# Performance work log

Measured on AMD Instinct MI355X. Metric: run time of the kernel, lower is better.

## Reference

```python
import jax, jax.numpy as jnp
import numpy as np

B, L, E, H = 8, 2048, 1024, 16
D = E // H
EPS = 1e-6


def setup_inputs() -> dict:
    key = jax.random.key(0)
    ks = jax.random.split(key, 9)
    s = 1.0 / np.sqrt(E)
    def lin_w(k):
        return jax.random.uniform(k, (E, E), jnp.float32, -s, s)
    def lin_b(k):
        return jax.random.uniform(k, (E,), jnp.float32, -s, s)
    return {
        "query": jax.random.normal(ks[0], (B, L, E), jnp.float32),
        "Wq": lin_w(ks[1]), "bq": lin_b(ks[2]),
        "Wk": lin_w(ks[3]), "bk": lin_b(ks[4]),
        "Wv": lin_w(ks[5]), "bv": lin_b(ks[6]),
        "Wo": lin_w(ks[7]), "bo": lin_b(ks[8]),
    }


def reference(query, Wq, bq, Wk, bk, Wv, bv, Wo, bo):
    bsz, tgt_len, embed_dim = query.shape
    n_head = H
    head_dim = embed_dim // n_head
    m = tgt_len  # src_len == tgt_len (self-attention)

    # projections (torch Linear with W stored as (in, out) here)
    q = query @ Wq + bq
    k = query @ Wk + bk
    v = query @ Wv + bv

    # (B, L, E) -> (B, H, L, D), softmax feature map over head dim
    def to_heads(x):
        return x.reshape(bsz, tgt_len, n_head, head_dim).transpose(0, 2, 1, 3)

    q = jax.nn.softmax(to_heads(q), axis=-1)
    k = jax.nn.softmax(to_heads(k), axis=-1)
    v = to_heads(v)
    comp_q = 1.0 - q
    comp_k = 1.0 - k

    # cosFormer positional reweighting: idx = (pi/2) * (1..m) / m
    idx = (np.pi / 2) * jnp.arange(1, m + 1, dtype=jnp.float32) / m  # (L,)
    sin = jnp.sin(idx)[None, None, :, None]  # (1,1,L,1)
    cos = jnp.cos(idx)[None, None, :, None]

    def feat(x):  # (B,H,L,D) -> (B,H,L,2D)
        return jnp.concatenate([x * sin, x * cos], axis=-1)

    qf, comp_qf = feat(q), feat(comp_q)
    kf, comp_kf = feat(k), feat(comp_k)

    def branch(qf_, kf_):
        kv = jnp.einsum('bhld,bhlm->bhdm', kf_, v)            # (B,H,2D,D)
        z = 1.0 / jnp.maximum(
            jnp.einsum('bhld,bhd->bhl', qf_, kf_.sum(axis=2)), EPS)
        return jnp.einsum('bhld,bhdm,bhl->bhlm', qf_, kv, z)  # (B,H,L,D)

    attn = branch(qf, kf) + branch(comp_qf, comp_kf)

    # torch: (B*H,L,D).transpose(0,1).view(L,B,E)
    out = attn.transpose(2, 0, 1, 3).reshape(tgt_len, bsz, embed_dim)
    out = out @ Wo + bo
    # torch final: .view(bsz, tgt_len, n_feat) -- raw reshape, no transpose
    return out.reshape(bsz, tgt_len, embed_dim)
```

## Files before the change

### kernel.cpp

```cpp
#include <hip/hip_runtime.h>
#include <hip/hip_bf16.h>
#include <cstdint>

#define B_   8
#define L_   2048
#define E_   1024
#define H_   16
#define D_   64
#define M_   (B_ * L_)
#define EPS_ 1e-6f
#define PI2_ 1.57079632679f

typedef __bf16 bf16;
typedef __bf16 bf16x8 __attribute__((ext_vector_type(8)));
typedef __bf16 bf16x4 __attribute__((ext_vector_type(4)));
typedef float  floatx4 __attribute__((ext_vector_type(4)));

__device__ inline void async_cp16(const void* g, void* l) {
  __builtin_amdgcn_global_load_lds(
      (__attribute__((address_space(1))) void*)const_cast<void*>(g),
      (__attribute__((address_space(3))) void*)l,
      16, 0, 0);
}

__global__ __launch_bounds__(256) void k_convert_x(const float* __restrict__ x,
                                                   bf16* __restrict__ o) {
  size_t i = ((size_t)blockIdx.x * 256 + threadIdx.x) * 8;
  floatx4 a = *(const floatx4*)(x + i);
  floatx4 b = *(const floatx4*)(x + i + 4);
  bf16x8 r;
  r[0] = (bf16)a[0]; r[1] = (bf16)a[1]; r[2] = (bf16)a[2]; r[3] = (bf16)a[3];
  r[4] = (bf16)b[0]; r[5] = (bf16)b[1]; r[6] = (bf16)b[2]; r[7] = (bf16)b[3];
  *(bf16x8*)(o + i) = r;
}

struct TArgs { const float* src[4]; bf16* dst[4]; };

__global__ __launch_bounds__(256) void k_transpose_w(TArgs t) {
  __shared__ float tile[32][33];
  const float* src = t.src[blockIdx.z];
  bf16* dst = t.dst[blockIdx.z];
  int bx = blockIdx.x, by = blockIdx.y;
  int x = threadIdx.x, y = threadIdx.y;
#pragma unroll
  for (int i = 0; i < 4; i++) {
    int r = by * 32 + y + i * 8;
    tile[y + i * 8][x] = src[(size_t)r * E_ + bx * 32 + x];
  }
  __syncthreads();
#pragma unroll
  for (int i = 0; i < 4; i++) {
    int r = bx * 32 + y + i * 8;
    dst[(size_t)r * E_ + by * 32 + x] = (bf16)tile[x][y + i * 8];
  }
}

#define BAR()   asm volatile("s_barrier" ::: "memory")
#define LGKM0() asm volatile("s_waitcnt lgkmcnt(0)" ::: "memory")
#define VMW4()  asm volatile("s_waitcnt vmcnt(4)" ::: "memory")
#define VMW0()  asm volatile("s_waitcnt vmcnt(0)" ::: "memory")
#define MFMA_   __builtin_amdgcn_mfma_f32_16x16x32_bf16

#define GEMM_TILE(t_, c_) {                                                    \
    const int t = (t_); const int c = (c_);                                    \
    bf16x8 a0[4][2], a1[4][2], b0[2][2], b1[2][2];                             \
                                                                  \
    _Pragma("unroll") for (int i = 0; i < 4; i++) {                            \
      a0[i][0] = RDA(c, 0, i); a0[i][1] = RDA(c, 1, i); }                      \
    _Pragma("unroll") for (int j = 0; j < 2; j++) {                            \
      b0[j][0] = RDB(c, 0, j); b0[j][1] = RDB(c, 1, j); }                      \
    if (t + 1 < 16) STAGE(c ^ 1, 0, t + 1, 0);                                 \
    BAR(); LGKM0();                                                            \
    __builtin_amdgcn_s_setprio(1);                                             \
    _Pragma("unroll") for (int i = 0; i < 4; i++)                              \
      _Pragma("unroll") for (int j = 0; j < 2; j++) {                          \
        acc[i][j] = MFMA_(a0[i][0], b0[j][0], acc[i][j], 0, 0, 0);             \
        acc[i][j] = MFMA_(a0[i][1], b0[j][1], acc[i][j], 0, 0, 0); }           \
    __builtin_amdgcn_s_setprio(0);                                             \
    BAR();                                                                     \
                                                                  \
    _Pragma("unroll") for (int j = 0; j < 2; j++) {                            \
      b1[j][0] = RDB(c, 0, j + 2); b1[j][1] = RDB(c, 1, j + 2); }              \
    if (t + 1 < 16) STAGE(c ^ 1, 0, t + 1, 1);                                 \
    BAR(); LGKM0();                                                            \
    __builtin_amdgcn_s_setprio(1);                                             \
    _Pragma("unroll") for (int i = 0; i < 4; i++)                              \
      _Pragma("unroll") for (int j = 0; j < 2; j++) {                          \
        acc[i][j + 2] = MFMA_(a0[i][0], b1[j][0], acc[i][j + 2], 0, 0, 0);     \
        acc[i][j + 2] = MFMA_(a0[i][1], b1[j][1], acc[i][j + 2], 0, 0, 0); }   \
    __builtin_amdgcn_s_setprio(0);                                             \
    BAR();                                                                     \
                                                                  \
    _Pragma("unroll") for (int i = 0; i < 4; i++) {                            \
      a1[i][0] = RDA(c, 0, i + 4); a1[i][1] = RDA(c, 1, i + 4); }              \
    if (t + 2 < 16) STAGE(c, 1, t + 2, 0);                                     \
    BAR(); LGKM0();                                                            \
    __builtin_amdgcn_s_setprio(1);                                             \
    _Pragma("unroll") for (int i = 0; i < 4; i++)                              \
      _Pragma("unroll") for (int j = 0; j < 2; j++) {                          \
        acc[i + 4][j + 2] = MFMA_(a1[i][0], b1[j][0], acc[i + 4][j + 2], 0, 0, 0); \
        acc[i + 4][j + 2] = MFMA_(a1[i][1], b1[j][1], acc[i + 4][j + 2], 0, 0, 0); } \
    __builtin_amdgcn_s_setprio(0);                                             \
    BAR();                                                                     \
                                                                  \
    if (t < 14) { STAGE(c, 1, t + 2, 1); VMW4(); } else { VMW0(); }            \
    BAR();                                                                     \
    __builtin_amdgcn_s_setprio(1);                                             \
    _Pragma("unroll") for (int i = 0; i < 4; i++)                              \
      _Pragma("unroll") for (int j = 0; j < 2; j++) {                          \
        acc[i + 4][j] = MFMA_(a1[i][0], b0[j][0], acc[i + 4][j], 0, 0, 0);     \
        acc[i + 4][j] = MFMA_(a1[i][1], b0[j][1], acc[i + 4][j], 0, 0, 0); }   \
    __builtin_amdgcn_s_setprio(0);                                             \
    BAR();                                                                     \
  }

__device__ __forceinline__ void gemm256_core(const bf16* __restrict__ Agl,
                                             const bf16* __restrict__ Bgl,
                                             int bm, int bn, bf16* ldsb,
                                             floatx4 (&acc)[8][4]) {
  const int tid  = threadIdx.x;
  const int wid  = tid >> 6;
  const int lane = tid & 63;
  const int quad = lane >> 4;
  const int l15  = lane & 15;
  const int wm   = wid >> 2;
  const int wn   = wid & 3;
  const int rb   = wn * 32;
  const int gcol = wm * 32 + (((lane & 3) * 8) ^ ((lane & 32) ? 16 : 0));
  const bf16* pA = Agl + (size_t)(bm * 256 + rb + (lane >> 2)) * E_ + gcol;
  const bf16* pB = Bgl + (size_t)(bn * 256 + rb + (lane >> 2)) * E_ + gcol;
  const int aCol = (quad * 8) ^ ((l15 & 8) ? 16 : 0);

  auto LDSP = [&](int c, int mat, int qq, int row, int col) -> bf16* {
    return ldsb + ((((c * 2 + mat) * 2 + qq) * 256 + row) * 32 + col);
  };
  auto STAGE = [&](int c, int mat, int tt, int h) {
    const bf16* g = (mat ? pB : pA) + (size_t)(h * 128) * E_ + tt * 64;
    bf16* lp = LDSP(c, mat, wm, h * 128 + rb, 0);
    async_cp16(g, lp);
    async_cp16(g + (size_t)16 * E_, lp + 16 * 32);
  };
  auto RDA = [&](int c, int qq, int i) -> bf16x8 {
    return *(const bf16x8*)LDSP(c, 0, qq, wm * 128 + i * 16 + l15, aCol);
  };
  auto RDB = [&](int c, int qq, int j) -> bf16x8 {
    return *(const bf16x8*)LDSP(c, 1, qq, wn * 64 + j * 16 + l15, aCol);
  };

  STAGE(0, 1, 0, 0); STAGE(0, 1, 0, 1);
  STAGE(0, 0, 0, 0); STAGE(0, 0, 0, 1);
  STAGE(1, 1, 1, 0); STAGE(1, 1, 1, 1);
  VMW4();
  BAR();

#pragma unroll 1
  for (int tb = 0; tb < 16; tb += 2) {
    GEMM_TILE(tb, 0)
    GEMM_TILE(tb + 1, 1)
  }
}

__global__ __launch_bounds__(512, 2) void k_gemm_qkv256(
    const bf16* __restrict__ A, const bf16* __restrict__ Wt,
    const float* __restrict__ bq, const float* __restrict__ bk,
    const float* __restrict__ bv,
    bf16* __restrict__ QTb, bf16* __restrict__ KTb, bf16* __restrict__ VT) {
  __shared__ __attribute__((aligned(16))) bf16 ldsb[2 * 2 * 2 * 256 * 32];
  const int id  = blockIdx.x;
  const int xcd = id & 7, rr = id >> 3;
  const int bm  = xcd * 8 + rr / 12;
  const int cz  = rr % 12;
  const int bn  = cz & 3, z = cz >> 2;
  const bf16* Bgl = Wt + (size_t)z * E_ * E_;

  floatx4 acc[8][4] = {};
  gemm256_core(A, Bgl, bm, bn, ldsb, acc);

  const int tid  = threadIdx.x;
  const int lane = tid & 63;
  const int wid  = tid >> 6;
  const int quad = lane >> 4;
  const int l15  = lane & 15;
  const int wm   = wid >> 2, wn = wid & 3;
  const float* bias = (z == 0) ? bq : (z == 1) ? bk : bv;
  float bb[4];
#pragma unroll
  for (int j = 0; j < 4; j++) bb[j] = bias[bn * 256 + wn * 64 + j * 16 + l15];

  if (z < 2) {
#pragma unroll
    for (int i = 0; i < 8; i++)
#pragma unroll
      for (int r = 0; r < 4; r++) {
        float v0 = acc[i][0][r] + bb[0];
        float v1 = acc[i][1][r] + bb[1];
        float v2 = acc[i][2][r] + bb[2];
        float v3 = acc[i][3][r] + bb[3];
        float m = fmaxf(fmaxf(v0, v1), fmaxf(v2, v3));
        m = fmaxf(m, __shfl_xor(m, 1));
        m = fmaxf(m, __shfl_xor(m, 2));
        m = fmaxf(m, __shfl_xor(m, 4));
        m = fmaxf(m, __shfl_xor(m, 8));
        v0 = __expf(v0 - m); v1 = __expf(v1 - m);
        v2 = __expf(v2 - m); v3 = __expf(v3 - m);
        float s = v0 + v1 + v2 + v3;
        s += __shfl_xor(s, 1); s += __shfl_xor(s, 2);
        s += __shfl_xor(s, 4); s += __shfl_xor(s, 8);
        const float inv = 1.f / s;
        acc[i][0][r] = v0 * inv; acc[i][1][r] = v1 * inv;
        acc[i][2][r] = v2 * inv; acc[i][3][r] = v3 * inv;
      }
  } else {
#pragma unroll
    for (int i = 0; i < 8; i++)
#pragma unroll
      for (int j = 0; j < 4; j++) {
        acc[i][j][0] += bb[j]; acc[i][j][1] += bb[j];
        acc[i][j][2] += bb[j]; acc[i][j][3] += bb[j];
      }
  }

  bf16* rep = ldsb;
#pragma unroll
  for (int i = 0; i < 8; i++)
#pragma unroll
    for (int j = 0; j < 4; j++) {
      const int c    = wn * 64 + j * 16 + l15;
      const int lrow = wm * 128 + i * 16 + quad * 4;
      bf16x4 rv;
      rv[0] = (bf16)acc[i][j][0]; rv[1] = (bf16)acc[i][j][1];
      rv[2] = (bf16)acc[i][j][2]; rv[3] = (bf16)acc[i][j][3];
      *(bf16x4*)&rep[(c * 256 + lrow) ^ ((c & 7) << 3)] = rv;
    }
  __syncthreads();

  bf16* OT = (z == 0) ? QTb : (z == 1) ? KTb : VT;
  const int b  = bm >> 3;
  const int lb = (bm & 7) * 256;
#pragma unroll
  for (int k = 0; k < 16; k++) {
    const int c   = k * 16 + (tid >> 5);
    const int lch = tid & 31;
    const int cg  = bn * 256 + c;
    bf16x8 v = *(const bf16x8*)&rep[(c * 256 + lch * 8) ^ ((c & 7) << 3)];
    *(bf16x8*)&OT[((size_t)((b * 16 + (cg >> 6)) * 64 + (cg & 63))) * 2048 + lb + lch * 8] = v;
  }
}

__global__ __launch_bounds__(512, 2) void k_gemm_final256(
    const bf16* __restrict__ A, const bf16* __restrict__ Bt,
    const float* __restrict__ bias, float* __restrict__ C) {
  __shared__ __attribute__((aligned(16))) bf16 ldsb[2 * 2 * 2 * 256 * 32];
  const int id  = blockIdx.x;
  const int xcd = id & 7, rr = id >> 3;
  const int bm  = xcd * 8 + (rr >> 2);
  const int bn  = rr & 3;

  floatx4 acc[8][4] = {};
  gemm256_core(A, Bt, bm, bn, ldsb, acc);

  const int tid  = threadIdx.x;
  const int wid  = tid >> 6;
  const int lane = tid & 63;
  const int quad = lane >> 4;
  const int l15  = lane & 15;
  const int wm   = wid >> 2, wn = wid & 3;
#pragma unroll
  for (int i = 0; i < 8; i++)
#pragma unroll
    for (int j = 0; j < 4; j++) {
      const int col = bn * 256 + wn * 64 + j * 16 + l15;
      const float bb = bias[col];
#pragma unroll
      for (int r = 0; r < 4; r++) {
        const int row = bm * 256 + wm * 128 + i * 16 + quad * 4 + r;
        C[(size_t)row * E_ + col] = acc[i][j][r] + bb;
      }
    }
}

__global__ __launch_bounds__(256) void k_kv(const bf16* __restrict__ KTb,
                                            const bf16* __restrict__ VT,
                                            float* __restrict__ kvp) {
  __shared__ __attribute__((aligned(16))) bf16 ktb[64 * 32];
  __shared__ __attribute__((aligned(16))) bf16 vt[64 * 32];
  __shared__ __attribute__((aligned(16))) bf16 Bsn[64 * 40];
  __shared__ __attribute__((aligned(16))) bf16 Bcs[64 * 40];
  __shared__ float snl[32], csl[32];
  const int kseg = blockIdx.x;
  const int bh   = blockIdx.y;
  const int t = threadIdx.x;
  const int wid = t >> 6, lane = t & 63;
  const int quad = lane >> 4, l15 = lane & 15;
  const int wm = wid >> 1, wn = wid & 1;

  const bf16* ktg = KTb + (size_t)bh * 64 * 2048;
  const bf16* vtg = VT  + (size_t)bh * 64 * 2048;

  floatx4 acc[4][2] = {};
  float rs = 0.f;
  const int d_ = t & 63, h_ = t >> 6;

  for (int it = 0; it < 16; it++) {
    const int l0 = kseg * 512 + it * 32;
    {
      const int r = lane >> 2, ch = lane & 3;
      const bf16* gk = ktg + (size_t)(wid * 16 + r) * 2048 + l0 + ((ch ^ (r & 1)) * 8);
      async_cp16(gk, &ktb[(wid * 16) * 32]);
      const bf16* gv = vtg + (size_t)(wid * 16 + r) * 2048 + l0 + ch * 8;
      async_cp16(gv, &vt[(wid * 16) * 32]);
    }
    if (t < 32) {
      const float ang = PI2_ * (float)(l0 + t + 1) / (float)L_;
      snl[t] = __sinf(ang); csl[t] = __cosf(ang);
    }
    __syncthreads();

    {
      const int row = t >> 2, cc = (t & 3) * 8;
      bf16x8 v = *(const bf16x8*)&vt[row * 32 + cc];
      bf16x8 a, b;
#pragma unroll
      for (int e = 0; e < 8; e++) {
        const float f = (float)v[e];
        a[e] = (bf16)(f * snl[cc + e]);
        b[e] = (bf16)(f * csl[cc + e]);
      }
      *(bf16x8*)&Bsn[row * 40 + cc] = a;
      *(bf16x8*)&Bcs[row * 40 + cc] = b;
    }
    if (t < 128) {
      float r8 = 0.f;
#pragma unroll
      for (int p = 0; p < 4; p++) {
        bf16x8 v = *(const bf16x8*)&ktb[d_ * 32 + p * 8];
        const int gl = (p ^ (d_ & 1)) * 8;
#pragma unroll
        for (int e = 0; e < 8; e++)
          r8 += (float)v[e] * (h_ ? csl[gl + e] : snl[gl + e]);
      }
      rs += r8;
    }
    __syncthreads();

    bf16x8 af[4], bfm[2];
    const bf16* Bsel = wm ? Bcs : Bsn;
#pragma unroll
    for (int i = 0; i < 4; i++)
      af[i] = *(const bf16x8*)&ktb[(i * 16 + l15) * 32 + ((quad ^ (l15 & 1)) * 8)];
#pragma unroll
    for (int j = 0; j < 2; j++)
      bfm[j] = *(const bf16x8*)&Bsel[(wn * 32 + j * 16 + l15) * 40 + quad * 8];
#pragma unroll
    for (int i = 0; i < 4; i++)
#pragma unroll
      for (int j = 0; j < 2; j++)
        acc[i][j] = __builtin_amdgcn_mfma_f32_16x16x32_bf16(af[i], bfm[j], acc[i][j], 0, 0, 0);
    __syncthreads();
  }

  float* C = kvp + (size_t)(kseg * 128 + bh) * 128 * 68;
#pragma unroll
  for (int i = 0; i < 4; i++)
#pragma unroll
    for (int j = 0; j < 2; j++) {
      const int col = wn * 32 + j * 16 + l15;
#pragma unroll
      for (int r = 0; r < 4; r++) {
        const int row = wm * 64 + i * 16 + quad * 4 + r;
        C[(size_t)row * 68 + col] = acc[i][j][r];
      }
    }
  if (t < 128) C[(size_t)t * 68 + 64] = rs;
}

__global__ __launch_bounds__(256) void k_consts(const float* __restrict__ kvp,
                                                bf16* __restrict__ KVT,
                                                float* __restrict__ ksbuf) {
  __shared__ float red[4][64];
  __shared__ float sksh[2];
  const int bh = blockIdx.x;
  const int t  = threadIdx.x;
  const int fq = t >> 6, dp = t & 63;
  const size_t gs = (size_t)128 * 128 * 68;
  const float* P = kvp + (size_t)bh * 128 * 68;
  bf16* kr = KVT + (size_t)(bh * 64 + dp) * 160;
  float sp = 0.f;
#pragma unroll 8
  for (int f = fq * 32; f < fq * 32 + 32; f++) {
    float v = P[(size_t)f * 68 + dp] + P[gs + (size_t)f * 68 + dp]
            + P[2 * gs + (size_t)f * 68 + dp] + P[3 * gs + (size_t)f * 68 + dp];
    kr[f] = (bf16)v;
    sp += v;
  }
  red[fq][dp] = sp;
  float ksv = 0.f;
  if (t < 128) {
    ksv = P[(size_t)t * 68 + 64] + P[gs + (size_t)t * 68 + 64]
        + P[2 * gs + (size_t)t * 68 + 64] + P[3 * gs + (size_t)t * 68 + 64];
    ksbuf[(size_t)bh * 136 + t] = ksv;
  }
  float sks = ksv;
#pragma unroll
  for (int o = 1; o < 64; o <<= 1) sks += __shfl_xor(sks, o);
  if (t == 0)  sksh[0] = sks;
  if (t == 64) sksh[1] = sks;
  __syncthreads();
  if (t < 64) {
    const float sk0 = red[0][t] + red[1][t];
    const float sk1 = red[2][t] + red[3][t];
    kr[128] = (bf16)(62.f * sk0);
    kr[129] = (bf16)(62.f * sk1);
#pragma unroll
    for (int f = 130; f < 160; f++) kr[f] = (bf16)0.f;
    if (t == 0) {
      ksbuf[(size_t)bh * 136 + 128] = sksh[0];
      ksbuf[(size_t)bh * 136 + 129] = sksh[1];
    }
  }
}

#define ASTR 168
__global__ __launch_bounds__(256) void k_attn(const bf16* __restrict__ QTb,
                                              const bf16* __restrict__ KVT,
                                              const float* __restrict__ ksbuf,
                                              bf16* __restrict__ attn) {
  __shared__ __attribute__((aligned(16))) bf16 Abuf[128 * ASTR];
  __shared__ __attribute__((aligned(16))) bf16 Bbuf[64 * ASTR];
  __shared__ float ksl[136];
  __shared__ float pth0[2][128], pth1[2][128];
  const int lc = blockIdx.x;
  const int bh = blockIdx.y;
  const int b = bh >> 4, h = bh & 15;
  const int t = threadIdx.x;

  {
    const bf16* src = KVT + (size_t)bh * 64 * 160;
#pragma unroll
    for (int i = 0; i < 5; i++) {
      const int idx = t + i * 256;
      const int row = idx / 20, ch = idx % 20;
      *(bf16x8*)&Bbuf[row * ASTR + ch * 8] = *(const bf16x8*)(src + row * 160 + ch * 8);
    }
    if (t < 130) ksl[t] = ksbuf[(size_t)bh * 136 + t];
  }
  __syncthreads();

  const int lr = t & 127, hf = t >> 7;
  const int l  = lc * 128 + lr;
  float xv[32];
  {
    const bf16* qp = QTb + (size_t)bh * 64 * 2048 + (size_t)(hf * 32) * 2048 + l;
#pragma unroll
    for (int d = 0; d < 32; d++) xv[d] = (float)qp[(size_t)d * 2048];
    float pa = 0.f, pb = 0.f;
#pragma unroll
    for (int d = 0; d < 32; d++) {
      pa += xv[d] * ksl[hf * 32 + d];
      pb += xv[d] * ksl[64 + hf * 32 + d];
    }
    pth0[hf][lr] = pa; pth1[hf][lr] = pb;
  }
  __syncthreads();

  {
    const float t0 = pth0[0][lr] + pth0[1][lr];
    const float t1 = pth1[0][lr] + pth1[1][lr];
    const float SKS0 = ksl[128], SKS1 = ksl[129];
    const float ang = PI2_ * (float)(l + 1) / (float)L_;
    const float sn = __sinf(ang), cs = __cosf(ang);
    const float den1 = sn * t0 + cs * t1;
    const float den2 = sn * (62.f * SKS0 + t0) + cs * (62.f * SKS1 + t1);
    const float z1 = 1.f / fmaxf(den1, EPS_);
    const float z2 = 1.f / fmaxf(den2, EPS_);
    const float zz = z1 + z2;
    const float a0 = zz * sn, a1 = zz * cs;
    bf16* ar = &Abuf[lr * ASTR];
#pragma unroll
    for (int g = 0; g < 4; g++) {
      bf16x8 w;
#pragma unroll
      for (int j = 0; j < 8; j++) w[j] = (bf16)(a0 * xv[g * 8 + j]);
      *(bf16x8*)(ar + hf * 32 + g * 8) = w;
    }
#pragma unroll
    for (int g = 0; g < 4; g++) {
      bf16x8 w;
#pragma unroll
      for (int j = 0; j < 8; j++) w[j] = (bf16)(a1 * xv[g * 8 + j]);
      *(bf16x8*)(ar + 64 + hf * 32 + g * 8) = w;
    }
    if (hf) {
      bf16x8 wt = {};
      wt[0] = (bf16)(z2 * sn); wt[1] = (bf16)(z2 * cs);
      *(bf16x8*)(ar + 128) = wt;
      bf16x8 zr = {};
      *(bf16x8*)(ar + 136) = zr;
      *(bf16x8*)(ar + 144) = zr;
      *(bf16x8*)(ar + 152) = zr;
    }
  }
  __syncthreads();

  const int wid = t >> 6, lane = t & 63;
  const int quad = lane >> 4, l15 = lane & 15;
  const int wm = wid >> 1, wn = wid & 1;
  floatx4 acc[4][2] = {};
#pragma unroll
  for (int kk = 0; kk < 5; kk++) {
    bf16x8 af[4], bfm[2];
#pragma unroll
    for (int i = 0; i < 4; i++)
      af[i] = *(const bf16x8*)&Abuf[(wm * 64 + i * 16 + l15) * ASTR + kk * 32 + quad * 8];
#pragma unroll
    for (int j = 0; j < 2; j++)
      bfm[j] = *(const bf16x8*)&Bbuf[(wn * 32 + j * 16 + l15) * ASTR + kk * 32 + quad * 8];
#pragma unroll
    for (int i = 0; i < 4; i++)
#pragma unroll
      for (int j = 0; j < 2; j++)
        acc[i][j] = __builtin_amdgcn_mfma_f32_16x16x32_bf16(af[i], bfm[j], acc[i][j], 0, 0, 0);
  }
#pragma unroll
  for (int i = 0; i < 4; i++)
#pragma unroll
    for (int j = 0; j < 2; j++) {
      const int dp = wn * 32 + j * 16 + l15;
#pragma unroll
      for (int r = 0; r < 4; r++) {
        const int lo = lc * 128 + wm * 64 + i * 16 + quad * 4 + r;
        attn[((size_t)lo * B_ + b) * E_ + h * 64 + dp] = (bf16)acc[i][j][r];
      }
    }
}

extern "C" void kernel_launch(void* const* d_in, const int* in_sizes, int n_in,
                              void* d_out, int out_size, void* d_ws, size_t ws_size,
                              hipStream_t stream) {
  (void)in_sizes; (void)n_in; (void)out_size; (void)ws_size;
  const float* query = (const float*)d_in[0];
  const float* Wq = (const float*)d_in[1];
  const float* bq = (const float*)d_in[2];
  const float* Wk = (const float*)d_in[3];
  const float* bk = (const float*)d_in[4];
  const float* Wv = (const float*)d_in[5];
  const float* bv = (const float*)d_in[6];
  const float* Wo = (const float*)d_in[7];
  const float* bo = (const float*)d_in[8];

  char* ws = (char*)d_ws;
  bf16*  QTb  = (bf16*) (ws + 0);
  bf16*  KTb  = (bf16*) (ws + 33554432);
  bf16*  VT   = (bf16*) (ws + 67108864);
  bf16*  Wt   = (bf16*) (ws + 100663296);
  bf16*  Xbf  = (bf16*) (ws + 109051904);
  bf16*  attnb= (bf16*) (ws + 109051904);
  float* kvp  = (float*)(ws + 142606336);
  bf16*  KVT  = (bf16*) (ws + 160432128);
  float* ksbuf= (float*)(ws + 163053568);

  k_convert_x<<<(M_ * E_) / (256 * 8), 256, 0, stream>>>(query, Xbf);

  TArgs ta;
  ta.src[0] = Wq; ta.src[1] = Wk; ta.src[2] = Wv; ta.src[3] = Wo;
  ta.dst[0] = Wt;                       ta.dst[1] = Wt + (size_t)E_ * E_;
  ta.dst[2] = Wt + (size_t)2 * E_ * E_; ta.dst[3] = Wt + (size_t)3 * E_ * E_;
  k_transpose_w<<<dim3(32, 32, 4), dim3(32, 8), 0, stream>>>(ta);

  k_gemm_qkv256<<<768, 512, 0, stream>>>(Xbf, Wt, bq, bk, bv, QTb, KTb, VT);

  k_kv<<<dim3(4, 128), 256, 0, stream>>>(KTb, VT, kvp);

  k_consts<<<128, 256, 0, stream>>>(kvp, KVT, ksbuf);

  k_attn<<<dim3(16, 128), 256, 0, stream>>>(QTb, KVT, ksbuf, attnb);

  k_gemm_final256<<<256, 512, 0, stream>>>(attnb, Wt + (size_t)3 * E_ * E_, bo, (float*)d_out);
}
```

Before: 351.1 us.

## Add nontemporal loads/stores, double-buffer k_kv, stage attn output through LDS, remap qkv grid

```diff
diff --git a/kernel.cpp b/kernel.cpp
--- a/kernel.cpp
+++ b/kernel.cpp
@@ -15,6 +15,7 @@
 typedef __bf16 bf16x8 __attribute__((ext_vector_type(8)));
 typedef __bf16 bf16x4 __attribute__((ext_vector_type(4)));
 typedef float  floatx4 __attribute__((ext_vector_type(4)));
+typedef unsigned int uintx4 __attribute__((ext_vector_type(4)));
 
 __device__ inline void async_cp16(const void* g, void* l) {
   __builtin_amdgcn_global_load_lds(
@@ -23,11 +24,20 @@
       16, 0, 0);
 }
 
+__device__ inline void nt_store16(bf16x8 v, bf16* p) {
+  __builtin_nontemporal_store(*(const uintx4*)&v, (uintx4*)p);
+}
+__device__ inline float ld_bf16_nt(const bf16* p) {
+  unsigned short s = __builtin_nontemporal_load((const unsigned short*)p);
+  unsigned int ui = (unsigned int)s << 16;
+  return __uint_as_float(ui);
+}
+
 __global__ __launch_bounds__(256) void k_convert_x(const float* __restrict__ x,
                                                    bf16* __restrict__ o) {
   size_t i = ((size_t)blockIdx.x * 256 + threadIdx.x) * 8;
-  floatx4 a = *(const floatx4*)(x + i);
-  floatx4 b = *(const floatx4*)(x + i + 4);
+  floatx4 a = __builtin_nontemporal_load(reinterpret_cast<const floatx4*>(x + i));
+  floatx4 b = __builtin_nontemporal_load(reinterpret_cast<const floatx4*>(x + i + 4));
   bf16x8 r;
   r[0] = (bf16)a[0]; r[1] = (bf16)a[1]; r[2] = (bf16)a[2]; r[3] = (bf16)a[3];
   r[4] = (bf16)b[0]; r[5] = (bf16)b[1]; r[6] = (bf16)b[2]; r[7] = (bf16)b[3];
@@ -168,8 +178,8 @@
   __shared__ __attribute__((aligned(16))) bf16 ldsb[2 * 2 * 2 * 256 * 32];
   const int id  = blockIdx.x;
   const int xcd = id & 7, rr = id >> 3;
-  const int bm  = xcd * 8 + rr / 12;
-  const int cz  = rr % 12;
+  const int bm  = xcd * 8 + (rr & 7);
+  const int cz  = rr >> 3;
   const int bn  = cz & 3, z = cz >> 2;
   const bf16* Bgl = Wt + (size_t)z * E_ * E_;
 
@@ -243,7 +253,7 @@
     const int lch = tid & 31;
     const int cg  = bn * 256 + c;
     bf16x8 v = *(const bf16x8*)&rep[(c * 256 + lch * 8) ^ ((c & 7) << 3)];
-    *(bf16x8*)&OT[((size_t)((b * 16 + (cg >> 6)) * 64 + (cg & 63))) * 2048 + lb + lch * 8] = v;
+    nt_store16(v, &OT[((size_t)((b * 16 + (cg >> 6)) * 64 + (cg & 63))) * 2048 + lb + lch * 8]);
   }
 }
 
@@ -274,7 +284,7 @@
 #pragma unroll
       for (int r = 0; r < 4; r++) {
         const int row = bm * 256 + wm * 128 + i * 16 + quad * 4 + r;
-        C[(size_t)row * E_ + col] = acc[i][j][r] + bb;
+        __builtin_nontemporal_store(acc[i][j][r] + bb, &C[(size_t)row * E_ + col]);
       }
     }
 }
@@ -282,11 +292,11 @@
 __global__ __launch_bounds__(256) void k_kv(const bf16* __restrict__ KTb,
                                             const bf16* __restrict__ VT,
                                             float* __restrict__ kvp) {
-  __shared__ __attribute__((aligned(16))) bf16 ktb[64 * 32];
-  __shared__ __attribute__((aligned(16))) bf16 vt[64 * 32];
+  __shared__ __attribute__((aligned(16))) bf16 ktb[2][64 * 32];
+  __shared__ __attribute__((aligned(16))) bf16 vt[2][64 * 32];
   __shared__ __attribute__((aligned(16))) bf16 Bsn[64 * 40];
   __shared__ __attribute__((aligned(16))) bf16 Bcs[64 * 40];
-  __shared__ float snl[32], csl[32];
+  __shared__ float snl[2][32], csl[2][32];
   const int kseg = blockIdx.x;
   const int bh   = blockIdx.y;
   const int t = threadIdx.x;
@@ -297,57 +307,70 @@
   const bf16* ktg = KTb + (size_t)bh * 64 * 2048;
   const bf16* vtg = VT  + (size_t)bh * 64 * 2048;
 
+  const int sr = lane >> 2, sch = lane & 3;
+
+  auto STG = [&](int it, int nb) {
+    const int l0 = kseg * 512 + it * 32;
+    const bf16* gk = ktg + (size_t)(wid * 16 + sr) * 2048 + l0 + ((sch ^ (sr & 1)) * 8);
+    async_cp16(gk, &ktb[nb][(wid * 16) * 32]);
+    const bf16* gv = vtg + (size_t)(wid * 16 + sr) * 2048 + l0 + sch * 8;
+    async_cp16(gv, &vt[nb][(wid * 16) * 32]);
+  };
+
   floatx4 acc[4][2] = {};
   float rs = 0.f;
   const int d_ = t & 63, h_ = t >> 6;
 
+  STG(0, 0);
+  if (t < 32) {
+    const float ang = PI2_ * (float)(kseg * 512 + t + 1) / (float)L_;
+    snl[0][t] = __sinf(ang); csl[0][t] = __cosf(ang);
+  }
+
   for (int it = 0; it < 16; it++) {
-    const int l0 = kseg * 512 + it * 32;
-    {
-      const int r = lane >> 2, ch = lane & 3;
-      const bf16* gk = ktg + (size_t)(wid * 16 + r) * 2048 + l0 + ((ch ^ (r & 1)) * 8);
-      async_cp16(gk, &ktb[(wid * 16) * 32]);
-      const bf16* gv = vtg + (size_t)(wid * 16 + r) * 2048 + l0 + ch * 8;
-      async_cp16(gv, &vt[(wid * 16) * 32]);
-    }
-    if (t < 32) {
-      const float ang = PI2_ * (float)(l0 + t + 1) / (float)L_;
-      snl[t] = __sinf(ang); csl[t] = __cosf(ang);
-    }
+    const int b = it & 1;
     __syncthreads();
+
+    if (it + 1 < 16) {
+      STG(it + 1, b ^ 1);
+      if (t < 32) {
+        const float ang = PI2_ * (float)(kseg * 512 + (it + 1) * 32 + t + 1) / (float)L_;
+        snl[(it + 1) & 1][t] = __sinf(ang); csl[(it + 1) & 1][t] = __cosf(ang);
+      }
+    }
 
     {
       const int row = t >> 2, cc = (t & 3) * 8;
-      bf16x8 v = *(const bf16x8*)&vt[row * 32 + cc];
-      bf16x8 a, b;
+      bf16x8 v = *(const bf16x8*)&vt[b][row * 32 + cc];
+      bf16x8 a, c;
 #pragma unroll
       for (int e = 0; e < 8; e++) {
         const float f = (float)v[e];
-        a[e] = (bf16)(f * snl[cc + e]);
-        b[e] = (bf16)(f * csl[cc + e]);
+        a[e] = (bf16)(f * snl[b][cc + e]);
+        c[e] = (bf16)(f * csl[b][cc + e]);
       }
       *(bf16x8*)&Bsn[row * 40 + cc] = a;
-      *(bf16x8*)&Bcs[row * 40 + cc] = b;
+      *(bf16x8*)&Bcs[row * 40 + cc] = c;
     }
     if (t < 128) {
       float r8 = 0.f;
 #pragma unroll
       for (int p = 0; p < 4; p++) {
-        bf16x8 v = *(const bf16x8*)&ktb[d_ * 32 + p * 8];
+        bf16x8 v = *(const bf16x8*)&ktb[b][d_ * 32 + p * 8];
         const int gl = (p ^ (d_ & 1)) * 8;
 #pragma unroll
         for (int e = 0; e < 8; e++)
-          r8 += (float)v[e] * (h_ ? csl[gl + e] : snl[gl + e]);
+          r8 += (float)v[e] * (h_ ? csl[b][gl + e] : snl[b][gl + e]);
       }
       rs += r8;
     }
-    __syncthreads();
+    LGKM0(); BAR();
 
     bf16x8 af[4], bfm[2];
     const bf16* Bsel = wm ? Bcs : Bsn;
 #pragma unroll
     for (int i = 0; i < 4; i++)
-      af[i] = *(const bf16x8*)&ktb[(i * 16 + l15) * 32 + ((quad ^ (l15 & 1)) * 8)];
+      af[i] = *(const bf16x8*)&ktb[b][(i * 16 + l15) * 32 + ((quad ^ (l15 & 1)) * 8)];
 #pragma unroll
     for (int j = 0; j < 2; j++)
       bfm[j] = *(const bf16x8*)&Bsel[(wn * 32 + j * 16 + l15) * 40 + quad * 8];
@@ -356,7 +379,6 @@
 #pragma unroll
       for (int j = 0; j < 2; j++)
         acc[i][j] = __builtin_amdgcn_mfma_f32_16x16x32_bf16(af[i], bfm[j], acc[i][j], 0, 0, 0);
-    __syncthreads();
   }
 
   float* C = kvp + (size_t)(kseg * 128 + bh) * 128 * 68;
@@ -368,10 +390,10 @@
 #pragma unroll
       for (int r = 0; r < 4; r++) {
         const int row = wm * 64 + i * 16 + quad * 4 + r;
-        C[(size_t)row * 68 + col] = acc[i][j][r];
-      }
-    }
-  if (t < 128) C[(size_t)t * 68 + 64] = rs;
+        __builtin_nontemporal_store(acc[i][j][r], &C[(size_t)row * 68 + col]);
+      }
+    }
+  if (t < 128) __builtin_nontemporal_store(rs, &C[(size_t)t * 68 + 64]);
 }
 
 __global__ __launch_bounds__(256) void k_consts(const float* __restrict__ kvp,
@@ -421,6 +443,7 @@
 }
 
 #define ASTR 168
+#define OSTR 72
 __global__ __launch_bounds__(256) void k_attn(const bf16* __restrict__ QTb,
                                               const bf16* __restrict__ KVT,
                                               const float* __restrict__ ksbuf,
@@ -452,7 +475,7 @@
   {
     const bf16* qp = QTb + (size_t)bh * 64 * 2048 + (size_t)(hf * 32) * 2048 + l;
 #pragma unroll
-    for (int d = 0; d < 32; d++) xv[d] = (float)qp[(size_t)d * 2048];
+    for (int d = 0; d < 32; d++) xv[d] = ld_bf16_nt(qp + (size_t)d * 2048);
     float pa = 0.f, pb = 0.f;
 #pragma unroll
     for (int d = 0; d < 32; d++) {
@@ -521,6 +544,9 @@
       for (int j = 0; j < 2; j++)
         acc[i][j] = __builtin_amdgcn_mfma_f32_16x16x32_bf16(af[i], bfm[j], acc[i][j], 0, 0, 0);
   }
+
+  __syncthreads();
+  bf16* ob = Abuf;
 #pragma unroll
   for (int i = 0; i < 4; i++)
 #pragma unroll
@@ -528,10 +554,20 @@
       const int dp = wn * 32 + j * 16 + l15;
 #pragma unroll
       for (int r = 0; r < 4; r++) {
-        const int lo = lc * 128 + wm * 64 + i * 16 + quad * 4 + r;
-        attn[((size_t)lo * B_ + b) * E_ + h * 64 + dp] = (bf16)acc[i][j][r];
-      }
-    }
+        const int ll = wm * 64 + i * 16 + quad * 4 + r;
+        ob[ll * OSTR + dp] = (bf16)acc[i][j][r];
+      }
+    }
+  __syncthreads();
+  {
+    const int ll = t >> 1, half = t & 1;
+    const size_t gbase = ((size_t)(lc * 128 + ll) * B_ + b) * E_ + h * 64 + half * 32;
+#pragma unroll
+    for (int g = 0; g < 4; g++) {
+      bf16x8 v = *(const bf16x8*)&ob[ll * OSTR + half * 32 + g * 8];
+      nt_store16(v, &attn[gbase + g * 8]);
+    }
+  }
 }
 
 extern "C" void kernel_launch(void* const* d_in, const int* in_sizes, int n_in,
```

Result: slower. 372.4 us (+6.1%).
